# Optimization experiments

Measured on AMD Instinct MI355X. Metric: run time of the kernel, lower is better.

## Reference

```python
import jax, jax.numpy as jnp
import numpy as np

B, T, D, H = 4, 2048, 1024, 16
HD = D // H  # head_dim = 64
SCALE = HD ** -0.5


def setup_inputs() -> dict:
    key = jax.random.key(0)
    k1, k2, k3 = jax.random.split(key, 3)
    x = jax.random.normal(k1, (B, T, D), dtype=jnp.float32)
    # xavier-uniform-like scaling for weights
    qkv_w = jax.random.normal(k2, (3 * D, D), dtype=jnp.float32) * (2.0 / (4 * D)) ** 0.5
    out_w = jax.random.normal(k3, (D, D), dtype=jnp.float32) * (1.0 / D) ** 0.5
    out_b = jnp.zeros((D,), dtype=jnp.float32)
    return {"x": x, "qkv_w": qkv_w, "out_w": out_w, "out_b": out_b}


def reference(x, qkv_w, out_w, out_b):
    Bx, Tx, _ = x.shape
    # qkv projection (nn.Linear: x @ W^T), no bias
    qkv = jnp.einsum('btd,ed->bte', x, qkv_w)  # [B,T,3D]
    qkv = qkv.reshape(Bx, Tx, 3, H, HD).transpose(2, 0, 3, 1, 4)  # [3,B,H,T,hd]
    q, k, v = qkv[0], qkv[1], qkv[2]
    scores = jnp.einsum('bhqd,bhkd->bhqk', q, k) * SCALE  # [B,H,T,T]
    causal = jnp.triu(jnp.ones((Tx, Tx), dtype=bool), k=1)
    scores = jnp.where(causal, -jnp.inf, scores)
    weights = jax.nn.softmax(scores, axis=-1)
    out = jnp.einsum('bhqk,bhkd->bhqd', weights, v)  # [B,H,T,hd]
    out = out.transpose(0, 2, 1, 3).reshape(Bx, Tx, D)
    return jnp.einsum('btd,ed->bte', out, out_w) + out_b
```

## Files before the change

kernel.cpp:

```cpp
#include <hip/hip_runtime.h>
#include <stdint.h>


typedef __bf16 bfx8 __attribute__((ext_vector_type(8)));
typedef float f32x4 __attribute__((ext_vector_type(4)));
typedef float f32x16 __attribute__((ext_vector_type(16)));

__device__ __forceinline__ uint16_t f2b(float f) {
  uint32_t u = __float_as_uint(f);
  u += 0x7fff + ((u >> 16) & 1);
  return (uint16_t)(u >> 16);
}

__device__ __forceinline__ uint32_t cvt_pk(float lo, float hi) {
  uint32_t r;
  asm("v_cvt_pk_bf16_f32 %0, %1, %2" : "=v"(r) : "v"(lo), "v"(hi));
  return r;
}

__device__ __forceinline__ void gld16(const void* g, void* l) {
  __builtin_amdgcn_global_load_lds((const __attribute__((address_space(1))) void*)g,
                                   (__attribute__((address_space(3))) void*)l,
                                   16, 0, 0);
}

__global__ __launch_bounds__(256) void cvt_bf16(const float* __restrict__ in,
                                                uint16_t* __restrict__ out, int n8) {
  int i = blockIdx.x * 256 + threadIdx.x;
  if (i >= n8) return;
  float4 a = ((const float4*)in)[2 * i];
  float4 b = ((const float4*)in)[2 * i + 1];
  union { uint16_t u[8]; uint4 v; } pk;
  pk.u[0] = f2b(a.x); pk.u[1] = f2b(a.y); pk.u[2] = f2b(a.z); pk.u[3] = f2b(a.w);
  pk.u[4] = f2b(b.x); pk.u[5] = f2b(b.y); pk.u[6] = f2b(b.z); pk.u[7] = f2b(b.w);
  ((uint4*)out)[i] = pk.v;
}

template <int OUTF32>
__global__ __launch_bounds__(256) void gemm_bt(const uint16_t* __restrict__ A,
                                               const uint16_t* __restrict__ B,
                                               void* __restrict__ Cout,
                                               const float* __restrict__ bias,
                                               int M, int N, int K, int nbx, int nwg) {
  __shared__ alignas(16) uint16_t As[2][128 * 32];
  __shared__ alignas(16) uint16_t Bs[2][128 * 32];

  int did = blockIdx.x;
  int wg = (did & 7) * (nwg >> 3) + (did >> 3);
  int bx = wg % nbx, by = wg / nbx;
  int m0 = by * 128, n0 = bx * 128;

  int tid = threadIdx.x;
  int lane = tid & 63, wid = tid >> 6;
  int wm = wid >> 1, wn = wid & 1;

  int rs = wid * 16 + (lane >> 2);
  int cs = (lane & 3) * 8;

  f32x4 acc[4][4] = {};

  auto stage = [&](int buf, int kt) {
    int k0 = kt * 32;
    gld16(&A[(size_t)(m0 + rs) * K + k0 + cs],      &As[buf][wid * 512]);
    gld16(&A[(size_t)(m0 + rs + 64) * K + k0 + cs], &As[buf][wid * 512 + 2048]);
    gld16(&B[(size_t)(n0 + rs) * K + k0 + cs],      &Bs[buf][wid * 512]);
    gld16(&B[(size_t)(n0 + rs + 64) * K + k0 + cs], &Bs[buf][wid * 512 + 2048]);
  };

  stage(0, 0);
  __syncthreads();

  int nk = K >> 5;
  int cur = 0;
  int ko = (lane >> 4) * 8;
  for (int kt = 0; kt < nk; ++kt) {
    if (kt + 1 < nk) stage(cur ^ 1, kt + 1);
    bfx8 a[4], b[4];
#pragma unroll
    for (int mi = 0; mi < 4; ++mi)
      a[mi] = *(const bfx8*)&As[cur][(wm * 64 + mi * 16 + (lane & 15)) * 32 + ko];
#pragma unroll
    for (int ni = 0; ni < 4; ++ni)
      b[ni] = *(const bfx8*)&Bs[cur][(wn * 64 + ni * 16 + (lane & 15)) * 32 + ko];
#pragma unroll
    for (int mi = 0; mi < 4; ++mi)
#pragma unroll
      for (int ni = 0; ni < 4; ++ni)
        acc[mi][ni] =
            __builtin_amdgcn_mfma_f32_16x16x32_bf16(a[mi], b[ni], acc[mi][ni], 0, 0, 0);
    __syncthreads();
    cur ^= 1;
  }

#pragma unroll
  for (int mi = 0; mi < 4; ++mi) {
    int row = m0 + wm * 64 + mi * 16 + ((lane >> 4) << 2);
#pragma unroll
    for (int ni = 0; ni < 4; ++ni) {
      int col = n0 + wn * 64 + ni * 16 + (lane & 15);
#pragma unroll
      for (int r = 0; r < 4; ++r) {
        float v = acc[mi][ni][r];
        if (OUTF32)
          ((float*)Cout)[(size_t)(row + r) * N + col] = v + bias[col];
        else
          ((uint16_t*)Cout)[(size_t)(row + r) * N + col] = f2b(v);
      }
    }
  }
}

__global__ __launch_bounds__(256, 3) void flash_attn(const uint16_t* __restrict__ qkv,
                                                     uint16_t* __restrict__ attnb) {
  const int T = 2048, D3 = 3072;
  const float CSC = 0.125f * 1.44269504f;
  __shared__ alignas(16) uint16_t Ks[2][64 * 64];
  __shared__ alignas(16) uint16_t Vt[3][64 * 64];

  int d = blockIdx.x;
  int bh = d & 63;
  int e = d >> 6;
  int hh = e >> 2, aa = e & 3;
  int qb = 4 * hh + ((aa + hh) & 3);
  int b = bh >> 4, h = bh & 15;
  int q0 = qb * 128;

  int tid = threadIdx.x, lane = tid & 63, wid = tid >> 6;
  int l31 = lane & 31, hi = lane >> 5;
  int qw = q0 + wid * 32;
  int swz = (lane & 7) << 3;

  size_t base = (size_t)b * T * D3;
  int hoff = h * 64;
  const uint16_t* kbase = &qkv[base + 1024 + hoff];
  const uint16_t* vbase = &qkv[base + 2048 + hoff];

  bfx8 qf[4];
  {
    const uint16_t* qp = &qkv[base + (size_t)(qw + l31) * D3 + hoff + 8 * hi];
#pragma unroll
    for (int h4 = 0; h4 < 4; ++h4) qf[h4] = *(const bfx8*)(qp + 16 * h4);
  }

  float mC = -1e30f, l_r = 0.f;
  f32x16 acc0 = {}, acc1 = {};
  bfx8 pf[4];
  int smax_prev = -1;
  int vb_prev = 0;

  int ntile = 2 * qb + 2;

  int krow = wid * 16 + (lane >> 3);
  int kc = ((lane & 7) << 3) ^ ((krow & 7) << 3);
  int vr = (tid & 31) * 2;
  int vc = (tid >> 5) * 8;
  uint4 vreg0, vreg1;

  auto loadV = [&](int kv0) {
    vreg0 = *(const uint4*)&vbase[(size_t)(kv0 + vr) * D3 + vc];
    vreg1 = *(const uint4*)&vbase[(size_t)(kv0 + vr + 1) * D3 + vc];
  };
  auto stageK = [&](int buf, int kv0) {
    gld16(&kbase[(size_t)(kv0 + krow) * D3 + kc], &Ks[buf][wid * 1024]);
    gld16(&kbase[(size_t)(kv0 + krow + 8) * D3 + kc], &Ks[buf][wid * 1024 + 512]);
  };
  auto writeV = [&](int vb) {
    union { uint4 v; uint16_t u[8]; } a, c;
    a.v = vreg0; c.v = vreg1;
#pragma unroll
    for (int j = 0; j < 8; ++j) {
      int hd = vc + j;
      uint32_t pk = (uint32_t)a.u[j] | ((uint32_t)c.u[j] << 16);
      *(uint32_t*)&Vt[vb][hd * 64 + (vr ^ ((hd & 7) << 3))] = pk;
    }
  };
  auto doPV = [&](int vb, int smx) {
    const uint16_t* vp = &Vt[vb][0];
    __builtin_amdgcn_s_setprio(1);
#pragma unroll
    for (int s = 0; s < 4; ++s) {
      if (s <= smx) {
        bfx8 v0 = *(const bfx8*)&vp[l31 * 64 + ((16 * s + 8 * hi) ^ swz)];
        acc0 = __builtin_amdgcn_mfma_f32_32x32x16_bf16(v0, pf[s], acc0, 0, 0, 0);
        bfx8 v1 = *(const bfx8*)&vp[(32 + l31) * 64 + ((16 * s + 8 * hi) ^ swz)];
        acc1 = __builtin_amdgcn_mfma_f32_32x32x16_bf16(v1, pf[s], acc1, 0, 0, 0);
      }
    }
    __builtin_amdgcn_s_setprio(0);
  };

  loadV(0);
  stageK(0, 0);
  writeV(0);
  __syncthreads();

  for (int kt = 0; kt < ntile; ++kt) {
    int kv0 = kt << 6;
    bool pre = (kt + 1 < ntile);
    if (pre) { loadV((kt + 1) << 6); stageK((kt + 1) & 1, (kt + 1) << 6); }

    int curK = kt & 1;
    bool active = (kv0 <= qw);
    int tmax = (qw > kv0) ? 2 : 1;
    f32x16 st0 = {}, st1 = {};

    if (active) {
      __builtin_amdgcn_s_setprio(1);
#pragma unroll
      for (int h4 = 0; h4 < 4; ++h4) {
        bfx8 kf0 = *(const bfx8*)&Ks[curK][l31 * 64 + ((16 * h4 + 8 * hi) ^ swz)];
        st0 = __builtin_amdgcn_mfma_f32_32x32x16_bf16(kf0, qf[h4], st0, 0, 0, 0);
        if (tmax == 2) {
          bfx8 kf1 = *(const bfx8*)&Ks[curK][(32 + l31) * 64 + ((16 * h4 + 8 * hi) ^ swz)];
          st1 = __builtin_amdgcn_mfma_f32_32x32x16_bf16(kf1, qf[h4], st1, 0, 0, 0);
        }
      }
      __builtin_amdgcn_s_setprio(0);
    }

    if (smax_prev >= 0) {
      doPV(vb_prev, smax_prev);
      smax_prev = -1;
    }

    if (active) {
      int q = qw + l31;
      float mx0 = -1e30f, mx1 = -1e30f;
      if (kv0 == qw) {
#pragma unroll
        for (int r = 0; r < 16; ++r) {
          int kv = kv0 + (r & 3) + 8 * (r >> 2) + 4 * hi;
          float v = st0[r];
          if (kv > q) v = -1e30f;
          st0[r] = v;
          mx0 = fmaxf(mx0, v);
        }
      } else {
#pragma unroll
        for (int r = 0; r < 16; ++r) mx0 = fmaxf(mx0, st0[r]);
      }
      if (tmax == 2) {
        if (kv0 + 32 == qw) {
#pragma unroll
          for (int r = 0; r < 16; ++r) {
            int kv = kv0 + 32 + (r & 3) + 8 * (r >> 2) + 4 * hi;
            float v = st1[r];
            if (kv > q) v = -1e30f;
            st1[r] = v;
            mx1 = fmaxf(mx1, v);
          }
        } else {
#pragma unroll
          for (int r = 0; r < 16; ++r) mx1 = fmaxf(mx1, st1[r]);
        }
      }
      float mS = fmaxf(mx0, mx1) * CSC;
      if (!__all(mS - mC <= 8.0f)) {
        float mSp = fmaxf(mS, __shfl_xor(mS, 32));
        float mCn = fmaxf(mC, mSp);
        float fac = __builtin_amdgcn_exp2f(mC - mCn);
        mC = mCn;
        l_r *= fac;
        acc0 *= fac;
        acc1 *= fac;
      }
      float l0 = 0.f, l1 = 0.f, l2 = 0.f, l3 = 0.f;
#pragma unroll
      for (int r = 0; r < 16; r += 4) {
        float e0 = __builtin_amdgcn_exp2f(fmaf(st0[r], CSC, -mC));
        float e1 = __builtin_amdgcn_exp2f(fmaf(st0[r + 1], CSC, -mC));
        float e2 = __builtin_amdgcn_exp2f(fmaf(st0[r + 2], CSC, -mC));
        float e3 = __builtin_amdgcn_exp2f(fmaf(st0[r + 3], CSC, -mC));
        st0[r] = e0; st0[r + 1] = e1; st0[r + 2] = e2; st0[r + 3] = e3;
        l0 += e0; l1 += e1; l2 += e2; l3 += e3;
      }
      if (tmax == 2) {
#pragma unroll
        for (int r = 0; r < 16; r += 4) {
          float e0 = __builtin_amdgcn_exp2f(fmaf(st1[r], CSC, -mC));
          float e1 = __builtin_amdgcn_exp2f(fmaf(st1[r + 1], CSC, -mC));
          float e2 = __builtin_amdgcn_exp2f(fmaf(st1[r + 2], CSC, -mC));
          float e3 = __builtin_amdgcn_exp2f(fmaf(st1[r + 3], CSC, -mC));
          st1[r] = e0; st1[r + 1] = e1; st1[r + 2] = e2; st1[r + 3] = e3;
          l0 += e0; l1 += e1; l2 += e2; l3 += e3;
        }
      }
      l_r += (l0 + l1) + (l2 + l3);

      int smax = (qw + 31 - kv0) >> 4;
      if (smax > 3) smax = 3;
#pragma unroll
      for (int s = 0; s < 4; ++s) {
        if (s <= smax) {
          int pb = 8 * (s & 1);
          uint32_t W0, W1, W2, W3;
          if (s < 2) {
            W0 = cvt_pk(st0[pb + 0], st0[pb + 1]);
            W1 = cvt_pk(st0[pb + 2], st0[pb + 3]);
            W2 = cvt_pk(st0[pb + 4], st0[pb + 5]);
            W3 = cvt_pk(st0[pb + 6], st0[pb + 7]);
          } else {
            W0 = cvt_pk(st1[pb + 0], st1[pb + 1]);
            W1 = cvt_pk(st1[pb + 2], st1[pb + 3]);
            W2 = cvt_pk(st1[pb + 4], st1[pb + 5]);
            W3 = cvt_pk(st1[pb + 6], st1[pb + 7]);
          }
          auto rA = __builtin_amdgcn_permlane32_swap(W0, W2, false, false);
          auto rB = __builtin_amdgcn_permlane32_swap(W1, W3, false, false);
          union { uint32_t u[4]; bfx8 v; } pk;
          pk.u[0] = rA[0]; pk.u[1] = rB[0]; pk.u[2] = rA[1]; pk.u[3] = rB[1];
          pf[s] = pk.v;
        }
      }
      smax_prev = smax;
      vb_prev = kt % 3;
    }

    if (pre) writeV((kt + 1) % 3);
    __syncthreads();
  }

  if (smax_prev >= 0) doPV(vb_prev, smax_prev);

  float l_tot = l_r + __shfl_xor(l_r, 32);
  __syncthreads();
  uint16_t* ow = ((uint16_t*)Ks) + wid * 2048;
  float rl = 1.0f / l_tot;
#pragma unroll
  for (int f = 0; f < 2; ++f) {
#pragma unroll
    for (int r = 0; r < 16; r += 2) {
      int hd = 32 * f + (r & 3) + 8 * (r >> 2) + 4 * hi;
      float v0 = (f ? acc1[r] : acc0[r]) * rl;
      float v1 = (f ? acc1[r + 1] : acc0[r + 1]) * rl;
      *(uint32_t*)&ow[l31 * 64 + (hd ^ ((l31 & 7) << 3))] = cvt_pk(v0, v1);
    }
  }
  __syncthreads();
  int row = lane >> 1, cb = (lane & 1) * 32;
  int q = q0 + wid * 32 + row;
  int rs = (row & 7) << 3;
  uint16_t* dst = &attnb[(size_t)(b * T + q) * 1024 + hoff + cb];
#pragma unroll
  for (int cc = 0; cc < 4; ++cc)
    *(uint4*)&dst[cc * 8] = *(const uint4*)&ow[row * 64 + ((cb + cc * 8) ^ rs)];
}

extern "C" void kernel_launch(void* const* d_in, const int* in_sizes, int n_in,
                              void* d_out, int out_size, void* d_ws, size_t ws_size,
                              hipStream_t stream) {
  const float* x = (const float*)d_in[0];
  const float* qkv_w = (const float*)d_in[1];
  const float* out_w = (const float*)d_in[2];
  const float* out_b = (const float*)d_in[3];
  float* out = (float*)d_out;

  char* ws = (char*)d_ws;
  uint16_t* xb    = (uint16_t*)(ws);
  uint16_t* qkvb  = (uint16_t*)(ws + 16777216);
  uint16_t* attnb = (uint16_t*)(ws + 67108864);
  uint16_t* wqkvb = (uint16_t*)(ws + 83886080);
  uint16_t* wob   = (uint16_t*)(ws + 90177536);

  cvt_bf16<<<4096, 256, 0, stream>>>(x, xb, 1048576);
  cvt_bf16<<<1536, 256, 0, stream>>>(qkv_w, wqkvb, 393216);
  cvt_bf16<<<512, 256, 0, stream>>>(out_w, wob, 131072);

  gemm_bt<0><<<1536, 256, 0, stream>>>(xb, wqkvb, (void*)qkvb, nullptr,
                                       8192, 3072, 1024, 24, 1536);
  flash_attn<<<1024, 256, 0, stream>>>(qkvb, attnb);
  gemm_bt<1><<<512, 256, 0, stream>>>(attnb, wob, (void*)out, out_b,
                                      8192, 1024, 1024, 8, 512);
}
```

Before: 197.3 us.

## Pair causal query blocks per workgroup and deepen K/V prefetch to two tiles

Each flash-attention workgroup now handles two query blocks, 15-a and a, so every block does the same total causal work, and the grid halves to 512. The K staging buffer grows to three slots and prefetch runs two tiles ahead. V is held in two alternating register pairs, with explicit waitcnt plus barrier replacing __syncthreads. Occupancy drops from 3 to 2 blocks per CU, and the extra LDS and registers reduce latency hiding from concurrent blocks.

```diff
diff --git a/kernel.cpp b/kernel.cpp
--- a/kernel.cpp
+++ b/kernel.cpp
@@ -110,24 +110,20 @@
   }
 }
 
-__global__ __launch_bounds__(256, 3) void flash_attn(const uint16_t* __restrict__ qkv,
+__global__ __launch_bounds__(256, 2) void flash_attn(const uint16_t* __restrict__ qkv,
                                                      uint16_t* __restrict__ attnb) {
   const int T = 2048, D3 = 3072;
   const float CSC = 0.125f * 1.44269504f;
-  __shared__ alignas(16) uint16_t Ks[2][64 * 64];
+  __shared__ alignas(16) uint16_t Ks[3][64 * 64];
   __shared__ alignas(16) uint16_t Vt[3][64 * 64];
 
   int d = blockIdx.x;
   int bh = d & 63;
-  int e = d >> 6;
-  int hh = e >> 2, aa = e & 3;
-  int qb = 4 * hh + ((aa + hh) & 3);
+  int a = d >> 6;
   int b = bh >> 4, h = bh & 15;
-  int q0 = qb * 128;
 
   int tid = threadIdx.x, lane = tid & 63, wid = tid >> 6;
   int l31 = lane & 31, hi = lane >> 5;
-  int qw = q0 + wid * 32;
   int swz = (lane & 7) << 3;
 
   size_t base = (size_t)b * T * D3;
@@ -135,215 +131,232 @@
   const uint16_t* kbase = &qkv[base + 1024 + hoff];
   const uint16_t* vbase = &qkv[base + 2048 + hoff];
 
-  bfx8 qf[4];
-  {
-    const uint16_t* qp = &qkv[base + (size_t)(qw + l31) * D3 + hoff + 8 * hi];
-#pragma unroll
-    for (int h4 = 0; h4 < 4; ++h4) qf[h4] = *(const bfx8*)(qp + 16 * h4);
-  }
-
-  float mC = -1e30f, l_r = 0.f;
-  f32x16 acc0 = {}, acc1 = {};
-  bfx8 pf[4];
-  int smax_prev = -1;
-  int vb_prev = 0;
-
-  int ntile = 2 * qb + 2;
-
   int krow = wid * 16 + (lane >> 3);
   int kc = ((lane & 7) << 3) ^ ((krow & 7) << 3);
   int vr = (tid & 31) * 2;
   int vc = (tid >> 5) * 8;
-  uint4 vreg0, vreg1;
-
-  auto loadV = [&](int kv0) {
-    vreg0 = *(const uint4*)&vbase[(size_t)(kv0 + vr) * D3 + vc];
-    vreg1 = *(const uint4*)&vbase[(size_t)(kv0 + vr + 1) * D3 + vc];
-  };
-  auto stageK = [&](int buf, int kv0) {
-    gld16(&kbase[(size_t)(kv0 + krow) * D3 + kc], &Ks[buf][wid * 1024]);
-    gld16(&kbase[(size_t)(kv0 + krow + 8) * D3 + kc], &Ks[buf][wid * 1024 + 512]);
-  };
-  auto writeV = [&](int vb) {
-    union { uint4 v; uint16_t u[8]; } a, c;
-    a.v = vreg0; c.v = vreg1;
-#pragma unroll
-    for (int j = 0; j < 8; ++j) {
-      int hd = vc + j;
-      uint32_t pk = (uint32_t)a.u[j] | ((uint32_t)c.u[j] << 16);
-      *(uint32_t*)&Vt[vb][hd * 64 + (vr ^ ((hd & 7) << 3))] = pk;
+
+  for (int p = 0; p < 2; ++p) {
+    int qb = (p == 0) ? (15 - a) : a;
+    int q0 = qb << 7;
+    int qw = q0 + wid * 32;
+    int ntile = 2 * qb + 2;
+
+    float mC = -1e30f, l_r = 0.f;
+    f32x16 acc0 = {}, acc1 = {};
+    bfx8 pf[4];
+    int smax_prev = -1, vb_prev = 0;
+
+    bfx8 qf[4];
+    {
+      const uint16_t* qp = &qkv[base + (size_t)(qw + l31) * D3 + hoff + 8 * hi];
+#pragma unroll
+      for (int h4 = 0; h4 < 4; ++h4) qf[h4] = *(const bfx8*)(qp + 16 * h4);
     }
-  };
-  auto doPV = [&](int vb, int smx) {
-    const uint16_t* vp = &Vt[vb][0];
-    __builtin_amdgcn_s_setprio(1);
-#pragma unroll
-    for (int s = 0; s < 4; ++s) {
-      if (s <= smx) {
-        bfx8 v0 = *(const bfx8*)&vp[l31 * 64 + ((16 * s + 8 * hi) ^ swz)];
-        acc0 = __builtin_amdgcn_mfma_f32_32x32x16_bf16(v0, pf[s], acc0, 0, 0, 0);
-        bfx8 v1 = *(const bfx8*)&vp[(32 + l31) * 64 + ((16 * s + 8 * hi) ^ swz)];
-        acc1 = __builtin_amdgcn_mfma_f32_32x32x16_bf16(v1, pf[s], acc1, 0, 0, 0);
-      }
+
+    uint4 vA0, vA1, vB0, vB1;
+
+    auto loadV = [&](int kv0, uint4& r0, uint4& r1) {
+      r0 = *(const uint4*)&vbase[(size_t)(kv0 + vr) * D3 + vc];
+      r1 = *(const uint4*)&vbase[(size_t)(kv0 + vr + 1) * D3 + vc];
+    };
+    auto stageK = [&](int buf, int kv0) {
+      gld16(&kbase[(size_t)(kv0 + krow) * D3 + kc], &Ks[buf][wid * 1024]);
+      gld16(&kbase[(size_t)(kv0 + krow + 8) * D3 + kc], &Ks[buf][wid * 1024 + 512]);
+    };
+    auto writeV = [&](int vb, const uint4& r0, const uint4& r1) {
+      union { uint4 v; uint16_t u[8]; } x, y;
+      x.v = r0; y.v = r1;
+#pragma unroll
+      for (int j = 0; j < 8; ++j) {
+        int hd = vc + j;
+        uint32_t pk = (uint32_t)x.u[j] | ((uint32_t)y.u[j] << 16);
+        *(uint32_t*)&Vt[vb][hd * 64 + (vr ^ ((hd & 7) << 3))] = pk;
+      }
+    };
+    auto doPV = [&]() {
+      const uint16_t* vp = &Vt[vb_prev][0];
+      __builtin_amdgcn_s_setprio(1);
+#pragma unroll
+      for (int s = 0; s < 4; ++s) {
+        if (s <= smax_prev) {
+          bfx8 v0 = *(const bfx8*)&vp[l31 * 64 + ((16 * s + 8 * hi) ^ swz)];
+          acc0 = __builtin_amdgcn_mfma_f32_32x32x16_bf16(v0, pf[s], acc0, 0, 0, 0);
+          bfx8 v1 = *(const bfx8*)&vp[(32 + l31) * 64 + ((16 * s + 8 * hi) ^ swz)];
+          acc1 = __builtin_amdgcn_mfma_f32_32x32x16_bf16(v1, pf[s], acc1, 0, 0, 0);
+        }
+      }
+      __builtin_amdgcn_s_setprio(0);
+    };
+
+    loadV(0, vA0, vA1);
+    stageK(0, 0);
+    writeV(0, vA0, vA1);
+    loadV(64, vB0, vB1);
+    stageK(1, 64);
+    asm volatile("s_waitcnt vmcnt(0) lgkmcnt(0)" ::: "memory");
+    __builtin_amdgcn_s_barrier();
+    __builtin_amdgcn_sched_barrier(0);
+
+    auto subiter = [&](int t, uint4& f0, uint4& f1, uint4& c0, uint4& c1) {
+      int kv0 = t << 6;
+      bool issue = (t + 2 < ntile);
+      if (issue) {
+        loadV((t + 2) << 6, f0, f1);
+        stageK((t + 2) % 3, (t + 2) << 6);
+      }
+      bool active = (kv0 <= qw);
+      int tmax = (qw > kv0) ? 2 : 1;
+      f32x16 st0 = {}, st1 = {};
+      if (active) {
+        const uint16_t* kp = &Ks[t % 3][0];
+        __builtin_amdgcn_s_setprio(1);
+#pragma unroll
+        for (int h4 = 0; h4 < 4; ++h4) {
+          bfx8 kf0 = *(const bfx8*)&kp[l31 * 64 + ((16 * h4 + 8 * hi) ^ swz)];
+          st0 = __builtin_amdgcn_mfma_f32_32x32x16_bf16(kf0, qf[h4], st0, 0, 0, 0);
+          if (tmax == 2) {
+            bfx8 kf1 = *(const bfx8*)&kp[(32 + l31) * 64 + ((16 * h4 + 8 * hi) ^ swz)];
+            st1 = __builtin_amdgcn_mfma_f32_32x32x16_bf16(kf1, qf[h4], st1, 0, 0, 0);
+          }
+        }
+        __builtin_amdgcn_s_setprio(0);
+      }
+
+      if (smax_prev >= 0) { doPV(); smax_prev = -1; }
+
+      if (active) {
+        int q = qw + l31;
+        float mx0 = -1e30f, mx1 = -1e30f;
+        if (kv0 == qw) {
+#pragma unroll
+          for (int r = 0; r < 16; ++r) {
+            int kv = kv0 + (r & 3) + 8 * (r >> 2) + 4 * hi;
+            float v = st0[r];
+            if (kv > q) v = -1e30f;
+            st0[r] = v;
+            mx0 = fmaxf(mx0, v);
+          }
+        } else {
+#pragma unroll
+          for (int r = 0; r < 16; ++r) mx0 = fmaxf(mx0, st0[r]);
+        }
+        if (tmax == 2) {
+          if (kv0 + 32 == qw) {
+#pragma unroll
+            for (int r = 0; r < 16; ++r) {
+              int kv = kv0 + 32 + (r & 3) + 8 * (r >> 2) + 4 * hi;
+              float v = st1[r];
+              if (kv > q) v = -1e30f;
+              st1[r] = v;
+              mx1 = fmaxf(mx1, v);
+            }
+          } else {
+#pragma unroll
+            for (int r = 0; r < 16; ++r) mx1 = fmaxf(mx1, st1[r]);
+          }
+        }
+        float mS = fmaxf(mx0, mx1) * CSC;
+        if (!__all(mS - mC <= 8.0f)) {
+          float mSp = fmaxf(mS, __shfl_xor(mS, 32));
+          float mCn = fmaxf(mC, mSp);
+          float fac = __builtin_amdgcn_exp2f(mC - mCn);
+          mC = mCn;
+          l_r *= fac;
+          acc0 *= fac;
+          acc1 *= fac;
+        }
+        float l0 = 0.f, l1 = 0.f, l2 = 0.f, l3 = 0.f;
+#pragma unroll
+        for (int r = 0; r < 16; r += 4) {
+          float e0 = __builtin_amdgcn_exp2f(fmaf(st0[r], CSC, -mC));
+          float e1 = __builtin_amdgcn_exp2f(fmaf(st0[r + 1], CSC, -mC));
+          float e2 = __builtin_amdgcn_exp2f(fmaf(st0[r + 2], CSC, -mC));
+          float e3 = __builtin_amdgcn_exp2f(fmaf(st0[r + 3], CSC, -mC));
+          st0[r] = e0; st0[r + 1] = e1; st0[r + 2] = e2; st0[r + 3] = e3;
+          l0 += e0; l1 += e1; l2 += e2; l3 += e3;
+        }
+        if (tmax == 2) {
+#pragma unroll
+          for (int r = 0; r < 16; r += 4) {
+            float e0 = __builtin_amdgcn_exp2f(fmaf(st1[r], CSC, -mC));
+            float e1 = __builtin_amdgcn_exp2f(fmaf(st1[r + 1], CSC, -mC));
+            float e2 = __builtin_amdgcn_exp2f(fmaf(st1[r + 2], CSC, -mC));
+            float e3 = __builtin_amdgcn_exp2f(fmaf(st1[r + 3], CSC, -mC));
+            st1[r] = e0; st1[r + 1] = e1; st1[r + 2] = e2; st1[r + 3] = e3;
+            l0 += e0; l1 += e1; l2 += e2; l3 += e3;
+          }
+        }
+        l_r += (l0 + l1) + (l2 + l3);
+
+        int smax = (qw + 31 - kv0) >> 4;
+        if (smax > 3) smax = 3;
+#pragma unroll
+        for (int s = 0; s < 4; ++s) {
+          if (s <= smax) {
+            int pb = 8 * (s & 1);
+            uint32_t W0, W1, W2, W3;
+            if (s < 2) {
+              W0 = cvt_pk(st0[pb + 0], st0[pb + 1]);
+              W1 = cvt_pk(st0[pb + 2], st0[pb + 3]);
+              W2 = cvt_pk(st0[pb + 4], st0[pb + 5]);
+              W3 = cvt_pk(st0[pb + 6], st0[pb + 7]);
+            } else {
+              W0 = cvt_pk(st1[pb + 0], st1[pb + 1]);
+              W1 = cvt_pk(st1[pb + 2], st1[pb + 3]);
+              W2 = cvt_pk(st1[pb + 4], st1[pb + 5]);
+              W3 = cvt_pk(st1[pb + 6], st1[pb + 7]);
+            }
+            auto rA = __builtin_amdgcn_permlane32_swap(W0, W2, false, false);
+            auto rB = __builtin_amdgcn_permlane32_swap(W1, W3, false, false);
+            union { uint32_t u[4]; bfx8 v; } pk;
+            pk.u[0] = rA[0]; pk.u[1] = rB[0]; pk.u[2] = rA[1]; pk.u[3] = rB[1];
+            pf[s] = pk.v;
+          }
+        }
+        smax_prev = smax;
+        vb_prev = t % 3;
+      }
+
+      if (t + 1 < ntile) writeV((t + 1) % 3, c0, c1);
+
+      if (issue)
+        asm volatile("s_waitcnt vmcnt(4) lgkmcnt(0)" ::: "memory");
+      else
+        asm volatile("s_waitcnt vmcnt(0) lgkmcnt(0)" ::: "memory");
+      __builtin_amdgcn_s_barrier();
+      __builtin_amdgcn_sched_barrier(0);
+    };
+
+    for (int t = 0; t < ntile; t += 2) {
+      subiter(t, vA0, vA1, vB0, vB1);
+      subiter(t + 1, vB0, vB1, vA0, vA1);
     }
-    __builtin_amdgcn_s_setprio(0);
-  };
-
-  loadV(0);
-  stageK(0, 0);
-  writeV(0);
-  __syncthreads();
-
-  for (int kt = 0; kt < ntile; ++kt) {
-    int kv0 = kt << 6;
-    bool pre = (kt + 1 < ntile);
-    if (pre) { loadV((kt + 1) << 6); stageK((kt + 1) & 1, (kt + 1) << 6); }
-
-    int curK = kt & 1;
-    bool active = (kv0 <= qw);
-    int tmax = (qw > kv0) ? 2 : 1;
-    f32x16 st0 = {}, st1 = {};
-
-    if (active) {
-      __builtin_amdgcn_s_setprio(1);
-#pragma unroll
-      for (int h4 = 0; h4 < 4; ++h4) {
-        bfx8 kf0 = *(const bfx8*)&Ks[curK][l31 * 64 + ((16 * h4 + 8 * hi) ^ swz)];
-        st0 = __builtin_amdgcn_mfma_f32_32x32x16_bf16(kf0, qf[h4], st0, 0, 0, 0);
-        if (tmax == 2) {
-          bfx8 kf1 = *(const bfx8*)&Ks[curK][(32 + l31) * 64 + ((16 * h4 + 8 * hi) ^ swz)];
-          st1 = __builtin_amdgcn_mfma_f32_32x32x16_bf16(kf1, qf[h4], st1, 0, 0, 0);
-        }
-      }
-      __builtin_amdgcn_s_setprio(0);
+    if (smax_prev >= 0) doPV();
+
+    float l_tot = l_r + __shfl_xor(l_r, 32);
+    __syncthreads();
+    uint16_t* ow = ((uint16_t*)Ks) + wid * 2048;
+    float rl = 1.0f / l_tot;
+#pragma unroll
+    for (int f = 0; f < 2; ++f) {
+#pragma unroll
+      for (int r = 0; r < 16; r += 2) {
+        int hd = 32 * f + (r & 3) + 8 * (r >> 2) + 4 * hi;
+        float v0 = (f ? acc1[r] : acc0[r]) * rl;
+        float v1 = (f ? acc1[r + 1] : acc0[r + 1]) * rl;
+        *(uint32_t*)&ow[l31 * 64 + (hd ^ ((l31 & 7) << 3))] = cvt_pk(v0, v1);
+      }
     }
-
-    if (smax_prev >= 0) {
-      doPV(vb_prev, smax_prev);
-      smax_prev = -1;
-    }
-
-    if (active) {
-      int q = qw + l31;
-      float mx0 = -1e30f, mx1 = -1e30f;
-      if (kv0 == qw) {
-#pragma unroll
-        for (int r = 0; r < 16; ++r) {
-          int kv = kv0 + (r & 3) + 8 * (r >> 2) + 4 * hi;
-          float v = st0[r];
-          if (kv > q) v = -1e30f;
-          st0[r] = v;
-          mx0 = fmaxf(mx0, v);
-        }
-      } else {
-#pragma unroll
-        for (int r = 0; r < 16; ++r) mx0 = fmaxf(mx0, st0[r]);
-      }
-      if (tmax == 2) {
-        if (kv0 + 32 == qw) {
-#pragma unroll
-          for (int r = 0; r < 16; ++r) {
-            int kv = kv0 + 32 + (r & 3) + 8 * (r >> 2) + 4 * hi;
-            float v = st1[r];
-            if (kv > q) v = -1e30f;
-            st1[r] = v;
-            mx1 = fmaxf(mx1, v);
-          }
-        } else {
-#pragma unroll
-          for (int r = 0; r < 16; ++r) mx1 = fmaxf(mx1, st1[r]);
-        }
-      }
-      float mS = fmaxf(mx0, mx1) * CSC;
-      if (!__all(mS - mC <= 8.0f)) {
-        float mSp = fmaxf(mS, __shfl_xor(mS, 32));
-        float mCn = fmaxf(mC, mSp);
-        float fac = __builtin_amdgcn_exp2f(mC - mCn);
-        mC = mCn;
-        l_r *= fac;
-        acc0 *= fac;
-        acc1 *= fac;
-      }
-      float l0 = 0.f, l1 = 0.f, l2 = 0.f, l3 = 0.f;
-#pragma unroll
-      for (int r = 0; r < 16; r += 4) {
-        float e0 = __builtin_amdgcn_exp2f(fmaf(st0[r], CSC, -mC));
-        float e1 = __builtin_amdgcn_exp2f(fmaf(st0[r + 1], CSC, -mC));
-        float e2 = __builtin_amdgcn_exp2f(fmaf(st0[r + 2], CSC, -mC));
-        float e3 = __builtin_amdgcn_exp2f(fmaf(st0[r + 3], CSC, -mC));
-        st0[r] = e0; st0[r + 1] = e1; st0[r + 2] = e2; st0[r + 3] = e3;
-        l0 += e0; l1 += e1; l2 += e2; l3 += e3;
-      }
-      if (tmax == 2) {
-#pragma unroll
-        for (int r = 0; r < 16; r += 4) {
-          float e0 = __builtin_amdgcn_exp2f(fmaf(st1[r], CSC, -mC));
-          float e1 = __builtin_amdgcn_exp2f(fmaf(st1[r + 1], CSC, -mC));
-          float e2 = __builtin_amdgcn_exp2f(fmaf(st1[r + 2], CSC, -mC));
-          float e3 = __builtin_amdgcn_exp2f(fmaf(st1[r + 3], CSC, -mC));
-          st1[r] = e0; st1[r + 1] = e1; st1[r + 2] = e2; st1[r + 3] = e3;
-          l0 += e0; l1 += e1; l2 += e2; l3 += e3;
-        }
-      }
-      l_r += (l0 + l1) + (l2 + l3);
-
-      int smax = (qw + 31 - kv0) >> 4;
-      if (smax > 3) smax = 3;
-#pragma unroll
-      for (int s = 0; s < 4; ++s) {
-        if (s <= smax) {
-          int pb = 8 * (s & 1);
-          uint32_t W0, W1, W2, W3;
-          if (s < 2) {
-            W0 = cvt_pk(st0[pb + 0], st0[pb + 1]);
-            W1 = cvt_pk(st0[pb + 2], st0[pb + 3]);
-            W2 = cvt_pk(st0[pb + 4], st0[pb + 5]);
-            W3 = cvt_pk(st0[pb + 6], st0[pb + 7]);
-          } else {
-            W0 = cvt_pk(st1[pb + 0], st1[pb + 1]);
-            W1 = cvt_pk(st1[pb + 2], st1[pb + 3]);
-            W2 = cvt_pk(st1[pb + 4], st1[pb + 5]);
-            W3 = cvt_pk(st1[pb + 6], st1[pb + 7]);
-          }
-          auto rA = __builtin_amdgcn_permlane32_swap(W0, W2, false, false);
-          auto rB = __builtin_amdgcn_permlane32_swap(W1, W3, false, false);
-          union { uint32_t u[4]; bfx8 v; } pk;
-          pk.u[0] = rA[0]; pk.u[1] = rB[0]; pk.u[2] = rA[1]; pk.u[3] = rB[1];
-          pf[s] = pk.v;
-        }
-      }
-      smax_prev = smax;
-      vb_prev = kt % 3;
-    }
-
-    if (pre) writeV((kt + 1) % 3);
+    int row = lane >> 1, cb = (lane & 1) * 32;
+    int q = q0 + wid * 32 + row;
+    int rs = (row & 7) << 3;
+    uint16_t* dst = &attnb[(size_t)(b * T + q) * 1024 + hoff + cb];
+#pragma unroll
+    for (int cc = 0; cc < 4; ++cc)
+      *(uint4*)&dst[cc * 8] = *(const uint4*)&ow[row * 64 + ((cb + cc * 8) ^ rs)];
     __syncthreads();
   }
-
-  if (smax_prev >= 0) doPV(vb_prev, smax_prev);
-
-  float l_tot = l_r + __shfl_xor(l_r, 32);
-  __syncthreads();
-  uint16_t* ow = ((uint16_t*)Ks) + wid * 2048;
-  float rl = 1.0f / l_tot;
-#pragma unroll
-  for (int f = 0; f < 2; ++f) {
-#pragma unroll
-    for (int r = 0; r < 16; r += 2) {
-      int hd = 32 * f + (r & 3) + 8 * (r >> 2) + 4 * hi;
-      float v0 = (f ? acc1[r] : acc0[r]) * rl;
-      float v1 = (f ? acc1[r + 1] : acc0[r + 1]) * rl;
-      *(uint32_t*)&ow[l31 * 64 + (hd ^ ((l31 & 7) << 3))] = cvt_pk(v0, v1);
-    }
-  }
-  __syncthreads();
-  int row = lane >> 1, cb = (lane & 1) * 32;
-  int q = q0 + wid * 32 + row;
-  int rs = (row & 7) << 3;
-  uint16_t* dst = &attnb[(size_t)(b * T + q) * 1024 + hoff + cb];
-#pragma unroll
-  for (int cc = 0; cc < 4; ++cc)
-    *(uint4*)&dst[cc * 8] = *(const uint4*)&ow[row * 64 + ((cb + cc * 8) ^ rs)];
 }
 
 extern "C" void kernel_launch(void* const* d_in, const int* in_sizes, int n_in,
@@ -368,7 +381,7 @@
 
   gemm_bt<0><<<1536, 256, 0, stream>>>(xb, wqkvb, (void*)qkvb, nullptr,
                                        8192, 3072, 1024, 24, 1536);
-  flash_attn<<<1024, 256, 0, stream>>>(qkvb, attnb);
+  flash_attn<<<512, 256, 0, stream>>>(qkvb, attnb);
   gemm_bt<1><<<512, 256, 0, stream>>>(attnb, wob, (void*)out, out_b,
                                       8192, 1024, 1024, 8, 512);
 }
```

Measured after the change: 193.9 us. About the same (-1.8%).
